# Optimization experiments

Measured on AMD Instinct MI355X. Metric: run time of the kernel, lower is better.

## Reference

```python
import jax, jax.numpy as jnp
import numpy as np

SHAPES = [38, 19, 10, 5, 3, 1]
SCALES = [0.1, 0.2, 0.375, 0.55, 0.725, 0.9, 1.075]
ASPECT_RATIOS = [[1.0, 2.0, 0.5], [1.0, 2.0, 0.5, 3.0, 0.3333],
                 [1.0, 2.0, 0.5, 3.0, 0.3333], [1.0, 2.0, 0.5, 3.0, 0.3333],
                 [1.0, 2.0, 0.5], [1.0, 2.0, 0.5]]
NUM_CONF = 21          # 20 foreground classes + 1 dummy/background
CONF_THRESH = 0.5
IOU_THRESH = 0.5


def gen_default_boxes():
    """SSD default boxes per level, stored as (cx, cy, h, w), shape [H, H, A, 4]."""
    out = []
    for k, H in enumerate(SHAPES):
        s, s_next = SCALES[k], SCALES[k + 1]
        hw = [(s / np.sqrt(ar), s * np.sqrt(ar)) for ar in ASPECT_RATIOS[k]]
        sp = np.sqrt(s * s_next)
        hw.append((sp, sp))
        hw = np.asarray(hw, np.float32)                      # [A, 2] (h, w)
        c = (np.arange(H, dtype=np.float32) + 0.5) / H
        cyg, cxg = np.meshgrid(c, c, indexing='ij')          # rows=cy, cols=cx
        A = hw.shape[0]
        db = np.empty((H, H, A, 4), np.float32)
        db[..., 0] = cxg[..., None]
        db[..., 1] = cyg[..., None]
        db[..., 2] = hw[:, 0]                                # h
        db[..., 3] = hw[:, 1]                                # w
        out.append(jnp.asarray(db))
    return out


def _decode_level(db, ft):
    coord = ft[..., :4]
    conf = jax.nn.softmax(ft[..., 4:], axis=-1)              # [B,H,W,A,21]
    cx = db[..., 0] + db[..., 3] * coord[..., 0]
    cy = db[..., 1] + db[..., 2] * coord[..., 1]
    h = db[..., 2] * jnp.exp(coord[..., 2])
    w = db[..., 3] * jnp.exp(coord[..., 3])
    box = jnp.stack([cx, cy, h, w], axis=-1)                 # cxcyhw
    conf_max = jnp.max(conf[..., :-1], axis=-1, keepdims=True)
    B = ft.shape[0]
    bwc = jnp.concatenate([box, conf_max], axis=-1).reshape(B, -1, 5)
    return bwc, conf.reshape(B, -1, NUM_CONF)


def _cxcyhw_to_xyxy(b):
    cx, cy, h, w = b[..., 0], b[..., 1], b[..., 2], b[..., 3]
    return jnp.stack([cx - w / 2, cy - h / 2, cx + w / 2, cy + h / 2], axis=-1)


def _pairwise_iou(a, b):
    lt = jnp.maximum(a[:, None, :2], b[None, :, :2])
    rb = jnp.minimum(a[:, None, 2:], b[None, :, 2:])
    wh = jnp.clip(rb - lt, 0.0)
    inter = wh[..., 0] * wh[..., 1]
    area_a = (a[:, 2] - a[:, 0]) * (a[:, 3] - a[:, 1])
    area_b = (b[:, 2] - b[:, 0]) * (b[:, 3] - b[:, 1])
    return inter / (area_a[:, None] + area_b[None, :] - inter + 1e-8)


def _nms_single(bwc, c):
    # bwc: [N, 5] (cxcyhw + max-conf), c: [N, 21]
    scores = bwc[:, 4]
    order = jnp.argsort(-scores)                             # descending
    sboxes = bwc[order, :4]
    sscores = scores[order]
    sconf = c[order]
    valid = sscores >= CONF_THRESH                           # conf filter as mask
    iou = _pairwise_iou(_cxcyhw_to_xyxy(sboxes), _cxcyhw_to_xyxy(sboxes))
    # torch: triu(1) < 0.5, then all over dim 0. Invalid (filtered) rows cannot suppress.
    ok = (jnp.triu(iou, k=1) < IOU_THRESH) | (~valid[:, None])
    keep = jnp.all(ok, axis=0) & valid
    km = keep[:, None].astype(sboxes.dtype)
    return jnp.concatenate([sboxes * km, sconf * km], axis=-1)  # [N, 25]


def setup_inputs() -> dict:
    key = jax.random.key(0)
    ks = jax.random.split(key, 6)
    B = 2
    A = [4, 6, 6, 6, 4, 4]
    inp = {}
    for i, (H, a) in enumerate(zip(SHAPES, A)):
        inp[f"f{i}"] = jax.random.normal(ks[i], (B, H, H, a, 4 + NUM_CONF), dtype=jnp.float32)
    return inp


def reference(f0, f1, f2, f3, f4, f5):
    feats = [f0, f1, f2, f3, f4, f5]
    dboxes = gen_default_boxes()
    bwc_all, conf_all = [], []
    for db, ft in zip(dboxes, feats):
        bwc, conf = _decode_level(db, ft)
        bwc_all.append(bwc)
        conf_all.append(conf)
    all_bwc = jnp.concatenate(bwc_all, axis=1)               # [B, 8732, 5]
    all_conf = jnp.concatenate(conf_all, axis=1)             # [B, 8732, 21]
    return jax.vmap(_nms_single)(all_bwc, all_conf)          # [B, 8732, 25]
```

## Files before the change

### kernel.cpp

```cpp
#include <hip/hip_runtime.h>
#include <math.h>

#define NBOX 8732
#define NCONF 21
#define NB 2
#define MAXV 2048
#define CONF_TH 0.5f
#define IOU_TH 0.5f
#define ENT_STRIDE 28

__device__ __constant__ int c_off[7] = {0, 5776, 7942, 8542, 8692, 8728, 8732};
__device__ __constant__ int c_H[6]   = {38, 19, 10, 5, 3, 1};
__device__ __constant__ int c_A[6]   = {4, 6, 6, 6, 4, 4};

__device__ inline void anchor_hw(int k, int a, float& h, float& w) {
    const double SC[7] = {0.1, 0.2, 0.375, 0.55, 0.725, 0.9, 1.075};
    int nar = (k >= 1 && k <= 3) ? 5 : 3;
    double s = SC[k], sn = SC[k + 1];
    if (a < nar) {
        double ar;
        switch (a) {
            case 0: ar = 1.0;    break;
            case 1: ar = 2.0;    break;
            case 2: ar = 0.5;    break;
            case 3: ar = 3.0;    break;
            default: ar = 0.3333; break;
        }
        double r = sqrt(ar);
        h = (float)(s / r);
        w = (float)(s * r);
    } else {
        float sp = (float)sqrt(s * sn);
        h = sp; w = sp;
    }
}

__global__ __launch_bounds__(256)
void decode_kernel(const float* __restrict__ f0, const float* __restrict__ f1,
                   const float* __restrict__ f2, const float* __restrict__ f3,
                   const float* __restrict__ f4, const float* __restrict__ f5,
                   unsigned int* __restrict__ counters,
                   float* __restrict__ entries) {
    int t = blockIdx.x * blockDim.x + threadIdx.x;
    if (t >= NB * NBOX) return;
    int b = t / NBOX;
    int n = t % NBOX;

    int k = 0;
    while (n >= c_off[k + 1]) ++k;
    int local = n - c_off[k];
    int A = c_A[k], H = c_H[k];
    int a = local % A;
    int cell = local / A;
    int x = cell % H;
    int y = cell / H;

    const float* f;
    switch (k) {
        case 0: f = f0; break; case 1: f = f1; break; case 2: f = f2; break;
        case 3: f = f3; break; case 4: f = f4; break; default: f = f5; break;
    }
    const float* p = f + ((((size_t)b * H + y) * H + x) * (size_t)A + a) * (4 + NCONF);

    float t0 = p[0], t1 = p[1], t2 = p[2], t3 = p[3];

    float lg[NCONF];
    float m = -1e30f;
#pragma unroll
    for (int c = 0; c < NCONF; c++) { lg[c] = p[4 + c]; m = fmaxf(m, lg[c]); }
    float sum = 0.f;
#pragma unroll
    for (int c = 0; c < NCONF; c++) { lg[c] = expf(lg[c] - m); sum += lg[c]; }
    float conf[NCONF];
#pragma unroll
    for (int c = 0; c < NCONF; c++) conf[c] = lg[c] / sum;
    float score = 0.f;
#pragma unroll
    for (int c = 0; c < NCONF - 1; c++) score = fmaxf(score, conf[c]);

    if (score >= CONF_TH) {
        float ah, aw;
        anchor_hw(k, a, ah, aw);
        float acx = ((float)x + 0.5f) / (float)H;
        float acy = ((float)y + 0.5f) / (float)H;
        float cx = acx + aw * t0;
        float cy = acy + ah * t1;
        float hh = ah * expf(t2);
        float ww = aw * expf(t3);

        unsigned int pos = atomicAdd(&counters[b], 1u);
        if (pos < MAXV) {
            float* e = entries + ((size_t)b * MAXV + pos) * ENT_STRIDE;
            e[0] = (float)n;
            e[1] = score;
            e[2] = cx; e[3] = cy; e[4] = hh; e[5] = ww;
#pragma unroll
            for (int c = 0; c < NCONF; c++) e[6 + c] = conf[c];
        }
    }
}

__global__ __launch_bounds__(256)
void nms_kernel(const unsigned int* __restrict__ counters,
                const float* __restrict__ entries,
                float* __restrict__ out) {
    int b = blockIdx.x;
    __shared__ float s_sc[MAXV];
    __shared__ int   s_id[MAXV];
    __shared__ float s_bx[MAXV][4];
    __shared__ short s_ord[MAXV];

    int K = (int)counters[b];
    if (K > MAXV) K = MAXV;

    for (int j = threadIdx.x; j < K; j += blockDim.x) {
        const float* e = entries + ((size_t)b * MAXV + j) * ENT_STRIDE;
        s_id[j] = (int)e[0];
        s_sc[j] = e[1];
        s_bx[j][0] = e[2]; s_bx[j][1] = e[3];
        s_bx[j][2] = e[4]; s_bx[j][3] = e[5];
    }
    __syncthreads();

    for (int j = threadIdx.x; j < K; j += blockDim.x) {
        float sj = s_sc[j];
        int   ij = s_id[j];
        int rank = 0;
        for (int i = 0; i < K; i++) {
            float si = s_sc[i];
            if (si > sj || (si == sj && s_id[i] < ij)) rank++;
        }
        s_ord[rank] = (short)j;
    }
    __syncthreads();

    for (int r = threadIdx.x; r < K; r += blockDim.x) {
        int j = s_ord[r];
        float cx = s_bx[j][0], cy = s_bx[j][1], hh = s_bx[j][2], ww = s_bx[j][3];
        float ax1 = cx - ww * 0.5f, ay1 = cy - hh * 0.5f;
        float ax2 = cx + ww * 0.5f, ay2 = cy + hh * 0.5f;
        float areaA = (ax2 - ax1) * (ay2 - ay1);
        bool sup = false;
        for (int q = 0; q < r && !sup; q++) {
            int i = s_ord[q];
            float icx = s_bx[i][0], icy = s_bx[i][1], ihh = s_bx[i][2], iww = s_bx[i][3];
            float bx1 = icx - iww * 0.5f, by1 = icy - ihh * 0.5f;
            float bx2 = icx + iww * 0.5f, by2 = icy + ihh * 0.5f;
            float lx = fmaxf(ax1, bx1), ly = fmaxf(ay1, by1);
            float rx = fminf(ax2, bx2), ry = fminf(ay2, by2);
            float iw = fmaxf(rx - lx, 0.f), ih = fmaxf(ry - ly, 0.f);
            float inter = iw * ih;
            float areaB = (bx2 - bx1) * (by2 - by1);
            float iou = inter / (areaA + areaB - inter + 1e-8f);
            if (iou >= IOU_TH) sup = true;
        }
        if (!sup) {
            float* o = out + ((size_t)b * NBOX + r) * (4 + NCONF);
            o[0] = cx; o[1] = cy; o[2] = hh; o[3] = ww;
            const float* e = entries + ((size_t)b * MAXV + j) * ENT_STRIDE;
#pragma unroll
            for (int c = 0; c < NCONF; c++) o[4 + c] = e[6 + c];
        }
    }
}

extern "C" void kernel_launch(void* const* d_in, const int* in_sizes, int n_in,
                              void* d_out, int out_size, void* d_ws, size_t ws_size,
                              hipStream_t stream) {
    const float* f0 = (const float*)d_in[0];
    const float* f1 = (const float*)d_in[1];
    const float* f2 = (const float*)d_in[2];
    const float* f3 = (const float*)d_in[3];
    const float* f4 = (const float*)d_in[4];
    const float* f5 = (const float*)d_in[5];

    unsigned int* counters = (unsigned int*)d_ws;
    float* entries = (float*)((char*)d_ws + 256);

    hipMemsetAsync(d_ws, 0, 256, stream);
    hipMemsetAsync(d_out, 0, (size_t)out_size * sizeof(float), stream);

    int total = NB * NBOX;
    int blocks = (total + 255) / 256;
    decode_kernel<<<blocks, 256, 0, stream>>>(f0, f1, f2, f3, f4, f5, counters, entries);
    nms_kernel<<<NB, 256, 0, stream>>>(counters, entries, (float*)d_out);
}
```

Before: 35.16 us.

## Fold memsets into decode, compact candidates in NMS block, recompute softmax for survivors

Two hipMemsetAsync calls go away: the output is zeroed inside the decode kernel, and the atomic counter now lives in shared memory. The decode kernel writes only a per-box score, and the NMS kernel compacts candidates from those scores. It then decodes boxes and recomputes softmax from the raw inputs only for boxes that survive, which avoids writing and reading the 28-float entry records. Candidate capacity drops from 2048 to 1024, so inputs with more confident boxes would be truncated. Candidate order now depends on shared-memory atomic order, but the rank sort uses ids as a tiebreak, so the result stays deterministic.

```diff
diff --git a/kernel.cpp b/kernel.cpp
--- a/kernel.cpp
+++ b/kernel.cpp
@@ -4,10 +4,11 @@
 #define NBOX 8732
 #define NCONF 21
 #define NB 2
-#define MAXV 2048
+#define MAXC 1024
 #define CONF_TH 0.5f
 #define IOU_TH 0.5f
-#define ENT_STRIDE 28
+#define NTOT (NB * NBOX)
+#define OUT_F4 (NTOT * 25 / 4)
 
 __device__ __constant__ int c_off[7] = {0, 5776, 7942, 8542, 8692, 8728, 8732};
 __device__ __constant__ int c_H[6]   = {38, 19, 10, 5, 3, 1};
@@ -35,17 +36,11 @@
     }
 }
 
-__global__ __launch_bounds__(256)
-void decode_kernel(const float* __restrict__ f0, const float* __restrict__ f1,
-                   const float* __restrict__ f2, const float* __restrict__ f3,
-                   const float* __restrict__ f4, const float* __restrict__ f5,
-                   unsigned int* __restrict__ counters,
-                   float* __restrict__ entries) {
-    int t = blockIdx.x * blockDim.x + threadIdx.x;
-    if (t >= NB * NBOX) return;
-    int b = t / NBOX;
-    int n = t % NBOX;
-
+__device__ inline const float* feat_ptr(int b, int n,
+                                        const float* f0, const float* f1,
+                                        const float* f2, const float* f3,
+                                        const float* f4, const float* f5,
+                                        int& k_out, int& a_out) {
     int k = 0;
     while (n >= c_off[k + 1]) ++k;
     int local = n - c_off[k];
@@ -54,71 +49,88 @@
     int cell = local / A;
     int x = cell % H;
     int y = cell / H;
-
     const float* f;
     switch (k) {
         case 0: f = f0; break; case 1: f = f1; break; case 2: f = f2; break;
         case 3: f = f3; break; case 4: f = f4; break; default: f = f5; break;
     }
-    const float* p = f + ((((size_t)b * H + y) * H + x) * (size_t)A + a) * (4 + NCONF);
-
-    float t0 = p[0], t1 = p[1], t2 = p[2], t3 = p[3];
+    k_out = k; a_out = a;
+    return f + ((((size_t)b * H + y) * H + x) * (size_t)A + a) * (4 + NCONF);
+}
+
+__global__ __launch_bounds__(256)
+void decode_kernel(const float* __restrict__ f0, const float* __restrict__ f1,
+                   const float* __restrict__ f2, const float* __restrict__ f3,
+                   const float* __restrict__ f4, const float* __restrict__ f5,
+                   float* __restrict__ scores, float4* __restrict__ out4) {
+    int t = blockIdx.x * blockDim.x + threadIdx.x;
+    int nthreads = gridDim.x * blockDim.x;
+
+    float4 z = make_float4(0.f, 0.f, 0.f, 0.f);
+    for (int i = t; i < OUT_F4; i += nthreads) out4[i] = z;
+
+    if (t >= NTOT) return;
+    int b = t / NBOX;
+    int n = t % NBOX;
+    int k, a;
+    const float* p = feat_ptr(b, n, f0, f1, f2, f3, f4, f5, k, a);
 
     float lg[NCONF];
     float m = -1e30f;
 #pragma unroll
     for (int c = 0; c < NCONF; c++) { lg[c] = p[4 + c]; m = fmaxf(m, lg[c]); }
-    float sum = 0.f;
-#pragma unroll
-    for (int c = 0; c < NCONF; c++) { lg[c] = expf(lg[c] - m); sum += lg[c]; }
-    float conf[NCONF];
-#pragma unroll
-    for (int c = 0; c < NCONF; c++) conf[c] = lg[c] / sum;
-    float score = 0.f;
-#pragma unroll
-    for (int c = 0; c < NCONF - 1; c++) score = fmaxf(score, conf[c]);
-
-    if (score >= CONF_TH) {
+    float sum = 0.f, maxfg = 0.f;
+#pragma unroll
+    for (int c = 0; c < NCONF; c++) {
+        float e = expf(lg[c] - m);
+        sum += e;
+        if (c < NCONF - 1) maxfg = fmaxf(maxfg, e);
+    }
+    scores[t] = maxfg / sum;
+}
+
+__global__ __launch_bounds__(256)
+void nms_kernel(const float* __restrict__ f0, const float* __restrict__ f1,
+                const float* __restrict__ f2, const float* __restrict__ f3,
+                const float* __restrict__ f4, const float* __restrict__ f5,
+                const float* __restrict__ scores, float* __restrict__ out) {
+    int b = blockIdx.x;
+    __shared__ int   s_cnt;
+    __shared__ float s_sc[MAXC];
+    __shared__ int   s_id[MAXC];
+    __shared__ float s_bx[MAXC][4];
+    __shared__ short s_ord[MAXC];
+
+    if (threadIdx.x == 0) s_cnt = 0;
+    __syncthreads();
+
+    for (int n = threadIdx.x; n < NBOX; n += blockDim.x) {
+        float s = scores[b * NBOX + n];
+        if (s >= CONF_TH) {
+            int pos = atomicAdd(&s_cnt, 1);
+            if (pos < MAXC) { s_sc[pos] = s; s_id[pos] = n; }
+        }
+    }
+    __syncthreads();
+    int K = s_cnt < MAXC ? s_cnt : MAXC;
+
+    for (int j = threadIdx.x; j < K; j += blockDim.x) {
+        int n = s_id[j];
+        int k, a;
+        const float* p = feat_ptr(b, n, f0, f1, f2, f3, f4, f5, k, a);
+        float t0 = p[0], t1 = p[1], t2 = p[2], t3 = p[3];
         float ah, aw;
         anchor_hw(k, a, ah, aw);
+        int local = n - c_off[k];
+        int H = c_H[k];
+        int cell = local / c_A[k];
+        int x = cell % H, y = cell / H;
         float acx = ((float)x + 0.5f) / (float)H;
         float acy = ((float)y + 0.5f) / (float)H;
-        float cx = acx + aw * t0;
-        float cy = acy + ah * t1;
-        float hh = ah * expf(t2);
-        float ww = aw * expf(t3);
-
-        unsigned int pos = atomicAdd(&counters[b], 1u);
-        if (pos < MAXV) {
-            float* e = entries + ((size_t)b * MAXV + pos) * ENT_STRIDE;
-            e[0] = (float)n;
-            e[1] = score;
-            e[2] = cx; e[3] = cy; e[4] = hh; e[5] = ww;
-#pragma unroll
-            for (int c = 0; c < NCONF; c++) e[6 + c] = conf[c];
-        }
-    }
-}
-
-__global__ __launch_bounds__(256)
-void nms_kernel(const unsigned int* __restrict__ counters,
-                const float* __restrict__ entries,
-                float* __restrict__ out) {
-    int b = blockIdx.x;
-    __shared__ float s_sc[MAXV];
-    __shared__ int   s_id[MAXV];
-    __shared__ float s_bx[MAXV][4];
-    __shared__ short s_ord[MAXV];
-
-    int K = (int)counters[b];
-    if (K > MAXV) K = MAXV;
-
-    for (int j = threadIdx.x; j < K; j += blockDim.x) {
-        const float* e = entries + ((size_t)b * MAXV + j) * ENT_STRIDE;
-        s_id[j] = (int)e[0];
-        s_sc[j] = e[1];
-        s_bx[j][0] = e[2]; s_bx[j][1] = e[3];
-        s_bx[j][2] = e[4]; s_bx[j][3] = e[5];
+        s_bx[j][0] = acx + aw * t0;
+        s_bx[j][1] = acy + ah * t1;
+        s_bx[j][2] = ah * expf(t2);
+        s_bx[j][3] = aw * expf(t3);
     }
     __syncthreads();
 
@@ -155,11 +167,20 @@
             if (iou >= IOU_TH) sup = true;
         }
         if (!sup) {
+            int n = s_id[j];
+            int k, a;
+            const float* p = feat_ptr(b, n, f0, f1, f2, f3, f4, f5, k, a);
             float* o = out + ((size_t)b * NBOX + r) * (4 + NCONF);
             o[0] = cx; o[1] = cy; o[2] = hh; o[3] = ww;
-            const float* e = entries + ((size_t)b * MAXV + j) * ENT_STRIDE;
-#pragma unroll
-            for (int c = 0; c < NCONF; c++) o[4 + c] = e[6 + c];
+            float lg[NCONF];
+            float m = -1e30f;
+#pragma unroll
+            for (int c = 0; c < NCONF; c++) { lg[c] = p[4 + c]; m = fmaxf(m, lg[c]); }
+            float sum = 0.f;
+#pragma unroll
+            for (int c = 0; c < NCONF; c++) { lg[c] = expf(lg[c] - m); sum += lg[c]; }
+#pragma unroll
+            for (int c = 0; c < NCONF; c++) o[4 + c] = lg[c] / sum;
         }
     }
 }
@@ -174,14 +195,11 @@
     const float* f4 = (const float*)d_in[4];
     const float* f5 = (const float*)d_in[5];
 
-    unsigned int* counters = (unsigned int*)d_ws;
-    float* entries = (float*)((char*)d_ws + 256);
-
-    hipMemsetAsync(d_ws, 0, 256, stream);
-    hipMemsetAsync(d_out, 0, (size_t)out_size * sizeof(float), stream);
-
-    int total = NB * NBOX;
-    int blocks = (total + 255) / 256;
-    decode_kernel<<<blocks, 256, 0, stream>>>(f0, f1, f2, f3, f4, f5, counters, entries);
-    nms_kernel<<<NB, 256, 0, stream>>>(counters, entries, (float*)d_out);
-}
+    float* scores = (float*)d_ws;
+
+    int blocks = (NTOT + 255) / 256;
+    decode_kernel<<<blocks, 256, 0, stream>>>(f0, f1, f2, f3, f4, f5,
+                                              scores, (float4*)d_out);
+    nms_kernel<<<NB, 256, 0, stream>>>(f0, f1, f2, f3, f4, f5,
+                                       scores, (float*)d_out);
+}
```

New measurement: 40.74 us. 15.9% more time.

## Fuse memsets, decode and NMS into one cooperative kernel with grid syncs

Applied to the files above, without the earlier changes.

Replaces two memsets and two kernel launches with a single cooperative-launched kernel that zeroes the counters and output, decodes boxes, and runs NMS, separated by grid-wide syncs. The aim is to remove launch and memset overhead between stages. It also cuts the candidate cap from 2048 to 1024 per batch to shrink shared memory, and defers the coordinate loads and per-class division until after the threshold test. Risks are grid-sync cost, and dropped candidates if more than 1024 boxes pass the threshold.

```diff
diff --git a/kernel.cpp b/kernel.cpp
--- a/kernel.cpp
+++ b/kernel.cpp
@@ -1,13 +1,19 @@
 #include <hip/hip_runtime.h>
+#include <hip/hip_cooperative_groups.h>
 #include <math.h>
+
+namespace cg = cooperative_groups;
 
 #define NBOX 8732
 #define NCONF 21
 #define NB 2
-#define MAXV 2048
+#define MAXC 1024
 #define CONF_TH 0.5f
 #define IOU_TH 0.5f
-#define ENT_STRIDE 28
+#define NTOT (NB * NBOX)
+#define OUT_F4 (NTOT * 25 / 4)
+#define GRID 69
+#define ENT 28
 
 __device__ __constant__ int c_off[7] = {0, 5776, 7942, 8542, 8692, 8728, 8732};
 __device__ __constant__ int c_H[6]   = {38, 19, 10, 5, 3, 1};
@@ -36,85 +42,91 @@
 }
 
 __global__ __launch_bounds__(256)
-void decode_kernel(const float* __restrict__ f0, const float* __restrict__ f1,
-                   const float* __restrict__ f2, const float* __restrict__ f3,
-                   const float* __restrict__ f4, const float* __restrict__ f5,
-                   unsigned int* __restrict__ counters,
-                   float* __restrict__ entries) {
-    int t = blockIdx.x * blockDim.x + threadIdx.x;
-    if (t >= NB * NBOX) return;
-    int b = t / NBOX;
-    int n = t % NBOX;
-
-    int k = 0;
-    while (n >= c_off[k + 1]) ++k;
-    int local = n - c_off[k];
-    int A = c_A[k], H = c_H[k];
-    int a = local % A;
-    int cell = local / A;
-    int x = cell % H;
-    int y = cell / H;
-
-    const float* f;
-    switch (k) {
-        case 0: f = f0; break; case 1: f = f1; break; case 2: f = f2; break;
-        case 3: f = f3; break; case 4: f = f4; break; default: f = f5; break;
-    }
-    const float* p = f + ((((size_t)b * H + y) * H + x) * (size_t)A + a) * (4 + NCONF);
-
-    float t0 = p[0], t1 = p[1], t2 = p[2], t3 = p[3];
-
-    float lg[NCONF];
-    float m = -1e30f;
-#pragma unroll
-    for (int c = 0; c < NCONF; c++) { lg[c] = p[4 + c]; m = fmaxf(m, lg[c]); }
-    float sum = 0.f;
-#pragma unroll
-    for (int c = 0; c < NCONF; c++) { lg[c] = expf(lg[c] - m); sum += lg[c]; }
-    float conf[NCONF];
-#pragma unroll
-    for (int c = 0; c < NCONF; c++) conf[c] = lg[c] / sum;
-    float score = 0.f;
-#pragma unroll
-    for (int c = 0; c < NCONF - 1; c++) score = fmaxf(score, conf[c]);
-
-    if (score >= CONF_TH) {
-        float ah, aw;
-        anchor_hw(k, a, ah, aw);
-        float acx = ((float)x + 0.5f) / (float)H;
-        float acy = ((float)y + 0.5f) / (float)H;
-        float cx = acx + aw * t0;
-        float cy = acy + ah * t1;
-        float hh = ah * expf(t2);
-        float ww = aw * expf(t3);
-
-        unsigned int pos = atomicAdd(&counters[b], 1u);
-        if (pos < MAXV) {
-            float* e = entries + ((size_t)b * MAXV + pos) * ENT_STRIDE;
-            e[0] = (float)n;
-            e[1] = score;
-            e[2] = cx; e[3] = cy; e[4] = hh; e[5] = ww;
-#pragma unroll
-            for (int c = 0; c < NCONF; c++) e[6 + c] = conf[c];
-        }
-    }
-}
-
-__global__ __launch_bounds__(256)
-void nms_kernel(const unsigned int* __restrict__ counters,
-                const float* __restrict__ entries,
-                float* __restrict__ out) {
-    int b = blockIdx.x;
-    __shared__ float s_sc[MAXV];
-    __shared__ int   s_id[MAXV];
-    __shared__ float s_bx[MAXV][4];
-    __shared__ short s_ord[MAXV];
-
+void fused_kernel(const float* __restrict__ f0, const float* __restrict__ f1,
+                  const float* __restrict__ f2, const float* __restrict__ f3,
+                  const float* __restrict__ f4, const float* __restrict__ f5,
+                  unsigned int* __restrict__ counters,
+                  float* __restrict__ entries,
+                  float* __restrict__ out) {
+    cg::grid_group gg = cg::this_grid();
+    const int tid = threadIdx.x;
+    const int bid = blockIdx.x;
+    const int t = bid * 256 + tid;
+    const int nthreads = GRID * 256;
+
+    __shared__ float s_sc[MAXC];
+    __shared__ int   s_id[MAXC];
+    __shared__ float s_bx[MAXC][4];
+    __shared__ short s_ord[MAXC];
+
+    if (t < 4) counters[t] = 0u;
+    float4 z = make_float4(0.f, 0.f, 0.f, 0.f);
+    float4* out4 = (float4*)out;
+    for (int i = t; i < OUT_F4; i += nthreads) out4[i] = z;
+
+    gg.sync();
+
+    if (t < NTOT) {
+        const int b = t / NBOX;
+        const int n = t % NBOX;
+        int k = 0;
+        while (n >= c_off[k + 1]) ++k;
+        const int local = n - c_off[k];
+        const int A = c_A[k], H = c_H[k];
+        const int a = local % A;
+        const int cell = local / A;
+        const int x = cell % H;
+        const int y = cell / H;
+        const float* f;
+        switch (k) {
+            case 0: f = f0; break; case 1: f = f1; break; case 2: f = f2; break;
+            case 3: f = f3; break; case 4: f = f4; break; default: f = f5; break;
+        }
+        const float* p = f + ((((size_t)b * H + y) * H + x) * (size_t)A + a) * (4 + NCONF);
+
+        float lg[NCONF];
+        float m = -1e30f;
+#pragma unroll
+        for (int c = 0; c < NCONF; c++) { lg[c] = p[4 + c]; m = fmaxf(m, lg[c]); }
+        float sum = 0.f, maxfg = 0.f;
+#pragma unroll
+        for (int c = 0; c < NCONF; c++) {
+            lg[c] = expf(lg[c] - m);
+            sum += lg[c];
+            if (c < NCONF - 1) maxfg = fmaxf(maxfg, lg[c]);
+        }
+        const float score = maxfg / sum;
+
+        if (score >= CONF_TH) {
+            float ah, aw;
+            anchor_hw(k, a, ah, aw);
+            const float acx = ((float)x + 0.5f) / (float)H;
+            const float acy = ((float)y + 0.5f) / (float)H;
+            const float t0 = p[0], t1 = p[1], t2 = p[2], t3 = p[3];
+            unsigned int pos = atomicAdd(&counters[b], 1u);
+            if (pos < MAXC) {
+                float* e = entries + ((size_t)b * MAXC + pos) * ENT;
+                e[0] = (float)n;
+                e[1] = score;
+                e[2] = acx + aw * t0;
+                e[3] = acy + ah * t1;
+                e[4] = ah * expf(t2);
+                e[5] = aw * expf(t3);
+#pragma unroll
+                for (int c = 0; c < NCONF; c++) e[6 + c] = lg[c] / sum;
+            }
+        }
+    }
+
+    gg.sync();
+
+    if (bid >= NB) return;
+    const int b = bid;
     int K = (int)counters[b];
-    if (K > MAXV) K = MAXV;
-
-    for (int j = threadIdx.x; j < K; j += blockDim.x) {
-        const float* e = entries + ((size_t)b * MAXV + j) * ENT_STRIDE;
+    if (K > MAXC) K = MAXC;
+
+    for (int j = tid; j < K; j += 256) {
+        const float* e = entries + ((size_t)b * MAXC + j) * ENT;
         s_id[j] = (int)e[0];
         s_sc[j] = e[1];
         s_bx[j][0] = e[2]; s_bx[j][1] = e[3];
@@ -122,42 +134,44 @@
     }
     __syncthreads();
 
-    for (int j = threadIdx.x; j < K; j += blockDim.x) {
-        float sj = s_sc[j];
-        int   ij = s_id[j];
+    for (int j = tid; j < K; j += 256) {
+        const float sj = s_sc[j];
+        const int   ij = s_id[j];
         int rank = 0;
         for (int i = 0; i < K; i++) {
-            float si = s_sc[i];
+            const float si = s_sc[i];
             if (si > sj || (si == sj && s_id[i] < ij)) rank++;
         }
         s_ord[rank] = (short)j;
     }
     __syncthreads();
 
-    for (int r = threadIdx.x; r < K; r += blockDim.x) {
-        int j = s_ord[r];
-        float cx = s_bx[j][0], cy = s_bx[j][1], hh = s_bx[j][2], ww = s_bx[j][3];
-        float ax1 = cx - ww * 0.5f, ay1 = cy - hh * 0.5f;
-        float ax2 = cx + ww * 0.5f, ay2 = cy + hh * 0.5f;
-        float areaA = (ax2 - ax1) * (ay2 - ay1);
+    for (int r = tid; r < K; r += 256) {
+        const int j = s_ord[r];
+        const float cx = s_bx[j][0], cy = s_bx[j][1];
+        const float hh = s_bx[j][2], ww = s_bx[j][3];
+        const float ax1 = cx - ww * 0.5f, ay1 = cy - hh * 0.5f;
+        const float ax2 = cx + ww * 0.5f, ay2 = cy + hh * 0.5f;
+        const float areaA = (ax2 - ax1) * (ay2 - ay1);
         bool sup = false;
         for (int q = 0; q < r && !sup; q++) {
-            int i = s_ord[q];
-            float icx = s_bx[i][0], icy = s_bx[i][1], ihh = s_bx[i][2], iww = s_bx[i][3];
-            float bx1 = icx - iww * 0.5f, by1 = icy - ihh * 0.5f;
-            float bx2 = icx + iww * 0.5f, by2 = icy + ihh * 0.5f;
-            float lx = fmaxf(ax1, bx1), ly = fmaxf(ay1, by1);
-            float rx = fminf(ax2, bx2), ry = fminf(ay2, by2);
-            float iw = fmaxf(rx - lx, 0.f), ih = fmaxf(ry - ly, 0.f);
-            float inter = iw * ih;
-            float areaB = (bx2 - bx1) * (by2 - by1);
-            float iou = inter / (areaA + areaB - inter + 1e-8f);
+            const int i = s_ord[q];
+            const float icx = s_bx[i][0], icy = s_bx[i][1];
+            const float ihh = s_bx[i][2], iww = s_bx[i][3];
+            const float bx1 = icx - iww * 0.5f, by1 = icy - ihh * 0.5f;
+            const float bx2 = icx + iww * 0.5f, by2 = icy + ihh * 0.5f;
+            const float lx = fmaxf(ax1, bx1), ly = fmaxf(ay1, by1);
+            const float rx = fminf(ax2, bx2), ry = fminf(ay2, by2);
+            const float iw = fmaxf(rx - lx, 0.f), ih = fmaxf(ry - ly, 0.f);
+            const float inter = iw * ih;
+            const float areaB = (bx2 - bx1) * (by2 - by1);
+            const float iou = inter / (areaA + areaB - inter + 1e-8f);
             if (iou >= IOU_TH) sup = true;
         }
         if (!sup) {
             float* o = out + ((size_t)b * NBOX + r) * (4 + NCONF);
             o[0] = cx; o[1] = cy; o[2] = hh; o[3] = ww;
-            const float* e = entries + ((size_t)b * MAXV + j) * ENT_STRIDE;
+            const float* e = entries + ((size_t)b * MAXC + j) * ENT;
 #pragma unroll
             for (int c = 0; c < NCONF; c++) o[4 + c] = e[6 + c];
         }
@@ -176,12 +190,12 @@
 
     unsigned int* counters = (unsigned int*)d_ws;
     float* entries = (float*)((char*)d_ws + 256);
-
-    hipMemsetAsync(d_ws, 0, 256, stream);
-    hipMemsetAsync(d_out, 0, (size_t)out_size * sizeof(float), stream);
-
-    int total = NB * NBOX;
-    int blocks = (total + 255) / 256;
-    decode_kernel<<<blocks, 256, 0, stream>>>(f0, f1, f2, f3, f4, f5, counters, entries);
-    nms_kernel<<<NB, 256, 0, stream>>>(counters, entries, (float*)d_out);
+    float* out = (float*)d_out;
+
+    void* args[] = {
+        (void*)&f0, (void*)&f1, (void*)&f2, (void*)&f3, (void*)&f4, (void*)&f5,
+        (void*)&counters, (void*)&entries, (void*)&out
+    };
+    hipLaunchCooperativeKernel((const void*)fused_kernel,
+                               dim3(GRID), dim3(256), args, 0, stream);
 }
```

Measured after the change: 59.04 us. 67.9% more time.
